# Kernel optimization log

Hardware: AMD Instinct MI355X
Metric: run time of the kernel (lower is better)

Reference implementation:

```python
import jax, jax.numpy as jnp
import numpy as np

K = 3          # kernel_size
A = 4          # spatial_atoms
PAD = (K - 1) // 2


def _unfold(x, k, pad):
    # torch F.unfold equivalent -> (B, C, k*k, H, W), taps ordered (kh, kw)
    B, C, H, W = x.shape
    xp = jnp.pad(x, ((0, 0), (0, 0), (pad, pad), (pad, pad)))
    taps = [xp[:, :, i:i + H, j:j + W] for i in range(k) for j in range(k)]
    return jnp.stack(taps, axis=2)


def setup_inputs() -> dict:
    key = jax.random.key(0)
    k1, k2, k3, k4 = jax.random.split(key, 4)
    B, C, O, H, W = 8, 64, 64, 64, 64
    x = jax.random.normal(k1, (B, C, H, W), dtype=jnp.float32)
    w_gen = jax.random.normal(k2, (O * A * K * K, C), dtype=jnp.float32) * 0.05
    b_gen = jax.random.normal(k3, (O * A * K * K,), dtype=jnp.float32) * 0.05
    pos_enc = jax.random.uniform(k4, (A, 2), dtype=jnp.float32, minval=-1.0, maxval=1.0)
    return {"x": x, "w_gen": w_gen, "b_gen": b_gen, "pos_enc": pos_enc}


def reference(x, w_gen, b_gen, pos_enc):
    B, C, H, W = x.shape
    O = w_gen.shape[0] // (A * K * K)

    # filter_gen: 1x1 conv + ReLU -> (B, O*A*K*K, H, W)
    filters = jnp.einsum('bchw,fc->bfhw', x, w_gen) + b_gen[None, :, None, None]
    filters = jax.nn.relu(filters)
    filters = filters.reshape(B, O, A, K * K, H, W)

    # position grid: stack((x_grid, y_grid)) with meshgrid indexing='ij'
    ys = jnp.linspace(-1.0, 1.0, H)
    xs = jnp.linspace(-1.0, 1.0, W)
    grid = jnp.stack(jnp.meshgrid(xs, ys, indexing='xy'), axis=-1)  # (H, W, 2)

    # spatial attention: (A, H, W)
    diff = grid[None] - pos_enc[:, None, None, :]
    att = jnp.exp(-jnp.sum(diff * diff, axis=-1))

    # combine atoms: (B, O, K*K, H, W)
    combined = jnp.einsum('boakhw,ahw->bokhw', filters, att)

    # unfold input and weighted sum over taps (valid since C == O)
    patches = _unfold(x, K, PAD)  # (B, C, K*K, H, W)
    out = jnp.sum(combined * patches, axis=2)  # (B, O, H, W)
    return out
```

## Files before the change

kernel.cpp:

```cpp
#include <hip/hip_runtime.h>
#include <math.h>

constexpr int NB = 8, NC = 64, NO = 64, NH = 64, NW = 64;

using f32x4 = __attribute__((ext_vector_type(4))) float;
using s16x8 = __attribute__((ext_vector_type(8))) short;
using u32x4 = __attribute__((ext_vector_type(4))) unsigned int;

__device__ __forceinline__ unsigned int pk2(float lo, float hi) {
    unsigned int r;
    asm("v_cvt_pk_bf16_f32 %0, %1, %2" : "=v"(r) : "v"(lo), "v"(hi));
    return r;
}
__device__ __forceinline__ unsigned short f2bf(float f) {
    unsigned u = __builtin_bit_cast(unsigned, f);
    return (unsigned short)((u + 0x7fffu + ((u >> 16) & 1u)) >> 16);
}
__device__ __forceinline__ float bf2f(unsigned short s) {
    unsigned u = ((unsigned)s) << 16;
    return __builtin_bit_cast(float, u);
}

__global__ __launch_bounds__(1024, 1)
void acda_kernel(const float* __restrict__ x, const float* __restrict__ w_gen,
                 const float* __restrict__ b_gen, const float* __restrict__ pos_enc,
                 float* __restrict__ out)
{
    __shared__ __align__(16) unsigned char arena[65536];
    __shared__ unsigned short Ws[16 * 36 * 64];
    __shared__ float BiasL[36 * 16];

    const int tid  = threadIdx.x;
    const int lane = tid & 63;
    const int wv   = tid >> 6;
    const int c0   = lane & 15, q = lane >> 4;
    const int hrow = wv >> 1, whalf = wv & 1;

    const int bx0  = blockIdx.x;
    const int xcd  = bx0 & 7;
    const int idx  = bx0 >> 3;
    const int osub = idx & 3;
    const int g    = xcd + 8 * (idx >> 2);
    const int b    = g >> 3;
    const int hoct = g & 7;
    const int hbase = hoct * 8;
    const int obase = osub * 16;
    const size_t xB = (size_t)b * NC * NH * NW;

    for (int u = tid; u < 4608; u += 1024) {
        const int o_l = u / 288;
        const int r   = u - o_l * 288;
        const int t   = r >> 3, cseg = r & 7;
        const float* src = w_gen + ((size_t)(obase + o_l) * 36 + t) * NC + cseg * 8;
        const float4 v0 = *reinterpret_cast<const float4*>(src);
        const float4 v1 = *reinterpret_cast<const float4*>(src + 4);
        u32x4 pk;
        pk[0] = pk2(v0.x, v0.y); pk[1] = pk2(v0.z, v0.w);
        pk[2] = pk2(v1.x, v1.y); pk[3] = pk2(v1.z, v1.w);
        const int byte = (o_l * 36 + t) * 128 + ((cseg * 16) ^ ((o_l & 7) << 4));
        *reinterpret_cast<u32x4*>(reinterpret_cast<char*>(Ws) + byte) = pk;
    }
    {
        const int w = lane;
#pragma unroll
        for (int i = 0; i < 4; ++i) {
            const int pair = wv * 4 + i;
            const int hs = pair >> 3, oct = pair & 7;
            const float* src = x + xB + (size_t)(oct * 8) * (NH * NW) + (hbase + hs) * NW + w;
            u32x4 pkv;
#pragma unroll
            for (int j = 0; j < 4; ++j)
                pkv[j] = pk2(src[(size_t)(2 * j) * (NH * NW)], src[(size_t)(2 * j + 1) * (NH * NW)]);
            const int loc  = hs * 64 + w;
            const int byte = loc * 128 + ((oct * 16) ^ ((loc & 7) << 4));
            *reinterpret_cast<u32x4*>(arena + byte) = pkv;
        }
    }
    for (int i = tid; i < 576; i += 1024) {
        const int t = i >> 4, o_l = i & 15;
        BiasL[i] = b_gen[(obase + o_l) * 36 + t];
    }
    __syncthreads();

    s16x8 xf[2][2];
#pragma unroll
    for (int nt = 0; nt < 2; ++nt) {
        const int loc = hrow * 64 + whalf * 32 + nt * 16 + c0;
#pragma unroll
        for (int kh2 = 0; kh2 < 2; ++kh2) {
            const int byte = loc * 128 + ((kh2 * 64 + q * 16) ^ ((loc & 7) << 4));
            xf[nt][kh2] = *reinterpret_cast<s16x8*>(arena + byte);
        }
    }
    __syncthreads();

    unsigned short* Patch = reinterpret_cast<unsigned short*>(arena);
    {
        const int o_l = tid >> 6, w = tid & 63;
        const float* xo = x + xB + (size_t)(obase + o_l) * (NH * NW);
#pragma unroll
        for (int hhi = 0; hhi < 10; ++hhi) {
            const int hh = hbase - 1 + hhi;
            const float v = (hh >= 0 && hh < NH) ? xo[hh * NW + w] : 0.0f;
            Patch[(hhi * 66 + w + 1) * 20 + o_l] = f2bf(v);
            if (w < 2) Patch[(hhi * 66 + (w ? 65 : 0)) * 20 + o_l] = 0;
        }
    }
    __syncthreads();

    const float gy = -1.0f + (2.0f / 63.0f) * (float)(hbase + hrow);
    float gxn[2];
#pragma unroll
    for (int nt = 0; nt < 2; ++nt)
        gxn[nt] = -1.0f + (2.0f / 63.0f) * (float)(whalf * 32 + nt * 16 + c0);

    const int wswz = (c0 & 7) << 4;
    const char* wrowp = reinterpret_cast<const char*>(Ws) + c0 * (36 * 128);

    float outacc[2][4] = {};

#pragma unroll
    for (int a = 0; a < 4; ++a) {
        float attn[2];
#pragma unroll
        for (int nt = 0; nt < 2; ++nt) {
            const float dx = gxn[nt] - pos_enc[2 * a], dy = gy - pos_enc[2 * a + 1];
            attn[nt] = __expf(-(dx * dx + dy * dy));
        }
#pragma unroll
        for (int k = 0; k < 9; ++k) {
            const int t  = a * 9 + k;
            const int kh = k / 3, kw = k - 3 * kh;
            const s16x8 wf0 = *reinterpret_cast<const s16x8*>(wrowp + t * 128 + ((q * 16) ^ wswz));
            const s16x8 wf1 = *reinterpret_cast<const s16x8*>(wrowp + t * 128 + ((64 + q * 16) ^ wswz));
            const f32x4 bb  = *reinterpret_cast<const f32x4*>(BiasL + t * 16 + q * 4);
#pragma unroll
            for (int nt = 0; nt < 2; ++nt) {
                f32x4 acc = bb;
                acc = __builtin_amdgcn_mfma_f32_16x16x32_bf16(wf0, xf[nt][0], acc, 0, 0, 0);
                acc = __builtin_amdgcn_mfma_f32_16x16x32_bf16(wf1, xf[nt][1], acc, 0, 0, 0);
                const ushort4 pu = *reinterpret_cast<const ushort4*>(
                    reinterpret_cast<const char*>(Patch) +
                    (((hrow + kh) * 66 + whalf * 32 + nt * 16 + c0 + kw) * 20 + q * 4) * 2);
                const float at = attn[nt];
                outacc[nt][0] = fmaf(fmaxf(acc[0], 0.f) * at, bf2f(pu.x), outacc[nt][0]);
                outacc[nt][1] = fmaf(fmaxf(acc[1], 0.f) * at, bf2f(pu.y), outacc[nt][1]);
                outacc[nt][2] = fmaf(fmaxf(acc[2], 0.f) * at, bf2f(pu.z), outacc[nt][2]);
                outacc[nt][3] = fmaf(fmaxf(acc[3], 0.f) * at, bf2f(pu.w), outacc[nt][3]);
            }
        }
    }

    const int h = hbase + hrow;
#pragma unroll
    for (int nt = 0; nt < 2; ++nt) {
        const int wcol = whalf * 32 + nt * 16 + c0;
#pragma unroll
        for (int r = 0; r < 4; ++r) {
            const int o = obase + q * 4 + r;
            out[(((size_t)b * NO + o) * NH + h) * NW + wcol] = outacc[nt][r];
        }
    }
}

extern "C" void kernel_launch(void* const* d_in, const int* in_sizes, int n_in,
                              void* d_out, int out_size, void* d_ws, size_t ws_size,
                              hipStream_t stream) {
    const float* x       = (const float*)d_in[0];
    const float* w_gen   = (const float*)d_in[1];
    const float* b_gen   = (const float*)d_in[2];
    const float* pos_enc = (const float*)d_in[3];
    float* out = (float*)d_out;

    dim3 grid(NB * 8 * 4);
    dim3 block(1024);
    hipLaunchKernelGGL(acda_kernel, grid, block, 0, stream,
                       x, w_gen, b_gen, pos_enc, out);
}
```

Baseline: 22.47 us.

## Split atoms across waves, halve rows per block, reduce via LDS

Each block now covers 4 rows instead of 8, which doubles the grid to 512 blocks. Within a block the 16 waves split the four atoms into two halves and combine their partial sums through shared memory before storing. The tap loop is reordered so attention-weighted filter sums over atoms are formed first and then multiplied once by the patch value, which cuts patch loads and FMAs. The trade-offs are a doubled per-block weight staging cost (Ws is reloaded by twice as many blocks), an extra barrier, and an LDS reduction.

```diff
diff --git a/kernel.cpp b/kernel.cpp
--- a/kernel.cpp
+++ b/kernel.cpp
@@ -26,24 +26,27 @@
                  const float* __restrict__ b_gen, const float* __restrict__ pos_enc,
                  float* __restrict__ out)
 {
-    __shared__ __align__(16) unsigned char arena[65536];
+    __shared__ unsigned short Xs[256 * 64];
     __shared__ unsigned short Ws[16 * 36 * 64];
+    __shared__ unsigned short Patch[6 * 66 * 20];
     __shared__ float BiasL[36 * 16];
 
     const int tid  = threadIdx.x;
     const int lane = tid & 63;
     const int wv   = tid >> 6;
     const int c0   = lane & 15, q = lane >> 4;
-    const int hrow = wv >> 1, whalf = wv & 1;
+    const int hrow  = wv >> 2;
+    const int ahalf = (wv >> 1) & 1;
+    const int whalf = wv & 1;
 
     const int bx0  = blockIdx.x;
     const int xcd  = bx0 & 7;
     const int idx  = bx0 >> 3;
     const int osub = idx & 3;
     const int g    = xcd + 8 * (idx >> 2);
-    const int b    = g >> 3;
-    const int hoct = g & 7;
-    const int hbase = hoct * 8;
+    const int b    = g >> 4;
+    const int hq   = g & 15;
+    const int hbase = hq * 4;
     const int obase = osub * 16;
     const size_t xB = (size_t)b * NC * NH * NW;
 
@@ -63,8 +66,8 @@
     {
         const int w = lane;
 #pragma unroll
-        for (int i = 0; i < 4; ++i) {
-            const int pair = wv * 4 + i;
+        for (int i = 0; i < 2; ++i) {
+            const int pair = wv * 2 + i;
             const int hs = pair >> 3, oct = pair & 7;
             const float* src = x + xB + (size_t)(oct * 8) * (NH * NW) + (hbase + hs) * NW + w;
             u32x4 pkv;
@@ -73,46 +76,54 @@
                 pkv[j] = pk2(src[(size_t)(2 * j) * (NH * NW)], src[(size_t)(2 * j + 1) * (NH * NW)]);
             const int loc  = hs * 64 + w;
             const int byte = loc * 128 + ((oct * 16) ^ ((loc & 7) << 4));
-            *reinterpret_cast<u32x4*>(arena + byte) = pkv;
-        }
-    }
-    for (int i = tid; i < 576; i += 1024) {
-        const int t = i >> 4, o_l = i & 15;
-        BiasL[i] = b_gen[(obase + o_l) * 36 + t];
-    }
-    __syncthreads();
-
-    s16x8 xf[2][2];
-#pragma unroll
-    for (int nt = 0; nt < 2; ++nt) {
-        const int loc = hrow * 64 + whalf * 32 + nt * 16 + c0;
-#pragma unroll
-        for (int kh2 = 0; kh2 < 2; ++kh2) {
-            const int byte = loc * 128 + ((kh2 * 64 + q * 16) ^ ((loc & 7) << 4));
-            xf[nt][kh2] = *reinterpret_cast<s16x8*>(arena + byte);
-        }
-    }
-    __syncthreads();
-
-    unsigned short* Patch = reinterpret_cast<unsigned short*>(arena);
+            *reinterpret_cast<u32x4*>(reinterpret_cast<char*>(Xs) + byte) = pkv;
+        }
+    }
     {
         const int o_l = tid >> 6, w = tid & 63;
         const float* xo = x + xB + (size_t)(obase + o_l) * (NH * NW);
 #pragma unroll
-        for (int hhi = 0; hhi < 10; ++hhi) {
+        for (int hhi = 0; hhi < 6; ++hhi) {
             const int hh = hbase - 1 + hhi;
             const float v = (hh >= 0 && hh < NH) ? xo[hh * NW + w] : 0.0f;
             Patch[(hhi * 66 + w + 1) * 20 + o_l] = f2bf(v);
-            if (w < 2) Patch[(hhi * 66 + (w ? 65 : 0)) * 20 + o_l] = 0;
-        }
+        }
+    }
+    if (tid < 192) {
+        const int hhi = tid >> 5, side = (tid >> 4) & 1, o_l = tid & 15;
+        Patch[(hhi * 66 + (side ? 65 : 0)) * 20 + o_l] = 0;
+    }
+    if (tid < 576) {
+        const int t = tid >> 4, o_l = tid & 15;
+        BiasL[tid] = b_gen[(obase + o_l) * 36 + t];
     }
     __syncthreads();
 
+    s16x8 xf[2][2];
+#pragma unroll
+    for (int nt = 0; nt < 2; ++nt) {
+        const int loc = hrow * 64 + whalf * 32 + nt * 16 + c0;
+#pragma unroll
+        for (int kh2 = 0; kh2 < 2; ++kh2) {
+            const int byte = loc * 128 + ((kh2 * 64 + q * 16) ^ ((loc & 7) << 4));
+            xf[nt][kh2] = *reinterpret_cast<s16x8*>(reinterpret_cast<char*>(Xs) + byte);
+        }
+    }
+    __syncthreads();
+
     const float gy = -1.0f + (2.0f / 63.0f) * (float)(hbase + hrow);
-    float gxn[2];
-#pragma unroll
-    for (int nt = 0; nt < 2; ++nt)
-        gxn[nt] = -1.0f + (2.0f / 63.0f) * (float)(whalf * 32 + nt * 16 + c0);
+    float attv[2][2];
+#pragma unroll
+    for (int a2 = 0; a2 < 2; ++a2) {
+        const int a = ahalf * 2 + a2;
+        const float px = pos_enc[2 * a], py = pos_enc[2 * a + 1];
+#pragma unroll
+        for (int nt = 0; nt < 2; ++nt) {
+            const float gx = -1.0f + (2.0f / 63.0f) * (float)(whalf * 32 + nt * 16 + c0);
+            const float dx = gx - px, dy = gy - py;
+            attv[a2][nt] = __expf(-(dx * dx + dy * dy));
+        }
+    }
 
     const int wswz = (c0 & 7) << 4;
     const char* wrowp = reinterpret_cast<const char*>(Ws) + c0 * (36 * 128);
@@ -120,17 +131,11 @@
     float outacc[2][4] = {};
 
 #pragma unroll
-    for (int a = 0; a < 4; ++a) {
-        float attn[2];
-#pragma unroll
-        for (int nt = 0; nt < 2; ++nt) {
-            const float dx = gxn[nt] - pos_enc[2 * a], dy = gy - pos_enc[2 * a + 1];
-            attn[nt] = __expf(-(dx * dx + dy * dy));
-        }
-#pragma unroll
-        for (int k = 0; k < 9; ++k) {
-            const int t  = a * 9 + k;
-            const int kh = k / 3, kw = k - 3 * kh;
+    for (int k = 0; k < 9; ++k) {
+        float tsum[2][4] = {};
+#pragma unroll
+        for (int a2 = 0; a2 < 2; ++a2) {
+            const int t = (ahalf * 2 + a2) * 9 + k;
             const s16x8 wf0 = *reinterpret_cast<const s16x8*>(wrowp + t * 128 + ((q * 16) ^ wswz));
             const s16x8 wf1 = *reinterpret_cast<const s16x8*>(wrowp + t * 128 + ((64 + q * 16) ^ wswz));
             const f32x4 bb  = *reinterpret_cast<const f32x4*>(BiasL + t * 16 + q * 4);
@@ -139,26 +144,46 @@
                 f32x4 acc = bb;
                 acc = __builtin_amdgcn_mfma_f32_16x16x32_bf16(wf0, xf[nt][0], acc, 0, 0, 0);
                 acc = __builtin_amdgcn_mfma_f32_16x16x32_bf16(wf1, xf[nt][1], acc, 0, 0, 0);
-                const ushort4 pu = *reinterpret_cast<const ushort4*>(
-                    reinterpret_cast<const char*>(Patch) +
-                    (((hrow + kh) * 66 + whalf * 32 + nt * 16 + c0 + kw) * 20 + q * 4) * 2);
-                const float at = attn[nt];
-                outacc[nt][0] = fmaf(fmaxf(acc[0], 0.f) * at, bf2f(pu.x), outacc[nt][0]);
-                outacc[nt][1] = fmaf(fmaxf(acc[1], 0.f) * at, bf2f(pu.y), outacc[nt][1]);
-                outacc[nt][2] = fmaf(fmaxf(acc[2], 0.f) * at, bf2f(pu.z), outacc[nt][2]);
-                outacc[nt][3] = fmaf(fmaxf(acc[3], 0.f) * at, bf2f(pu.w), outacc[nt][3]);
+                const float at = attv[a2][nt];
+#pragma unroll
+                for (int r = 0; r < 4; ++r)
+                    tsum[nt][r] = fmaf(at, fmaxf(acc[r], 0.f), tsum[nt][r]);
             }
         }
-    }
-
-    const int h = hbase + hrow;
-#pragma unroll
-    for (int nt = 0; nt < 2; ++nt) {
-        const int wcol = whalf * 32 + nt * 16 + c0;
-#pragma unroll
-        for (int r = 0; r < 4; ++r) {
-            const int o = obase + q * 4 + r;
-            out[(((size_t)b * NO + o) * NH + h) * NW + wcol] = outacc[nt][r];
+        const int kh = k / 3, kw = k - 3 * kh;
+#pragma unroll
+        for (int nt = 0; nt < 2; ++nt) {
+            const ushort4 pu = *reinterpret_cast<const ushort4*>(
+                reinterpret_cast<const char*>(Patch) +
+                (((hrow + kh) * 66 + whalf * 32 + nt * 16 + c0 + kw) * 20 + q * 4) * 2);
+            outacc[nt][0] = fmaf(tsum[nt][0], bf2f(pu.x), outacc[nt][0]);
+            outacc[nt][1] = fmaf(tsum[nt][1], bf2f(pu.y), outacc[nt][1]);
+            outacc[nt][2] = fmaf(tsum[nt][2], bf2f(pu.z), outacc[nt][2]);
+            outacc[nt][3] = fmaf(tsum[nt][3], bf2f(pu.w), outacc[nt][3]);
+        }
+    }
+
+    float* MB = reinterpret_cast<float*>(Xs);
+    const int slot = ((tid >> 8) << 7) | (tid & 127);
+    if (ahalf == 1) {
+        float* d = MB + slot * 8;
+#pragma unroll
+        for (int nt = 0; nt < 2; ++nt)
+#pragma unroll
+            for (int r = 0; r < 4; ++r) d[nt * 4 + r] = outacc[nt][r];
+    }
+    __syncthreads();
+    if (ahalf == 0) {
+        const float* s = MB + slot * 8;
+        const int h = hbase + hrow;
+#pragma unroll
+        for (int nt = 0; nt < 2; ++nt) {
+            const int wcol = whalf * 32 + nt * 16 + c0;
+#pragma unroll
+            for (int r = 0; r < 4; ++r) {
+                const int o = obase + q * 4 + r;
+                out[(((size_t)b * NO + o) * NH + h) * NW + wcol] = outacc[nt][r] + s[nt * 4 + r];
+            }
         }
     }
 }
@@ -172,7 +197,7 @@
     const float* pos_enc = (const float*)d_in[3];
     float* out = (float*)d_out;
 
-    dim3 grid(NB * 8 * 4);
+    dim3 grid(NB * 16 * 4);
     dim3 block(1024);
     hipLaunchKernelGGL(acda_kernel, grid, block, 0, stream,
                        x, w_gen, b_gen, pos_enc, out);
```

After: 59.86 us. 2.66x slower.
